# Performance work log

Hardware: AMD Instinct MI355X
Metric: run time of the kernel (lower is better)

## Reference

```python
import jax, jax.numpy as jnp
import numpy as np

B, U, T, H = 64, 64, 512, 8
N_NEIGHBORS = 8
NEG = -1e9

def setup_inputs() -> dict:
    key = jax.random.key(0)
    ks = jax.random.split(key, 12)
    f32 = jnp.float32
    def n(k, shp, s=1.0):
        return jax.random.normal(k, shp, dtype=f32) * s
    return {
        "usv_features": n(ks[0], (B, U, 4)),
        "task_features": n(ks[1], (B, T, 5)),
        "adj_matrix": jax.random.randint(ks[2], (B, U, T), 0, 2, dtype=jnp.int32),
        "edge_features": n(ks[3], (B, U, T, 1)),
        "W_usv": n(ks[4], (4, H), 0.3), "b_usv": jnp.zeros((H,), f32),
        "W_task": n(ks[5], (5, H), 0.3), "b_task": jnp.zeros((H,), f32),
        "W_au": n(ks[6], (H, 1), 0.3), "b_au": jnp.zeros((1,), f32),
        "W_at": n(ks[7], (H, 1), 0.3), "b_at": jnp.zeros((1,), f32),
        "W_Q": n(ks[8], (H, H), 0.3), "b_Q": jnp.zeros((H,), f32),
        "W_K": n(ks[9], (H, H), 0.3), "b_K": jnp.zeros((H,), f32),
        "W_V": n(ks[10], (H, H), 0.3), "b_V": jnp.zeros((H,), f32),
    }

def reference(usv_features, task_features, adj_matrix, edge_features,
              W_usv, b_usv, W_task, b_task, W_au, b_au, W_at, b_at,
              W_Q, b_Q, W_K, b_K, W_V, b_V):
    n_tasks = task_features.shape[1]
    # --- node encoders ---
    usv_embed = usv_features @ W_usv + b_usv        # [B,U,H]
    task_embed = task_features @ W_task + b_task    # [B,T,H]
    # --- USV <- Task additive attention ---
    uq = usv_embed @ W_Q + b_Q                      # [B,U,H]
    tk = task_embed @ W_K + b_K                     # [B,T,H]
    s = jnp.tanh(uq[:, :, None, :] + tk[:, None, :, :])  # [B,U,T,H]
    s = (s @ W_au + b_au)[..., 0]                   # [B,U,T]
    s = jnp.where(adj_matrix == 0, NEG, s)
    w = jax.nn.softmax(s, axis=-1)
    agg_task = jnp.einsum('but,bth->buh', w, task_embed)
    usv_self = jax.nn.sigmoid(uq)
    usv_updated = jax.nn.elu(usv_self * usv_embed + agg_task)  # [B,U,H]
    # --- Task <- Task kNN attention ---
    tq = task_embed @ W_V + b_V                     # [B,T,H]  (query via W_V as in source)
    coords = task_features[:, :, 0:2]
    diff = coords[:, :, None, :] - coords[:, None, :, :]
    dist = jnp.sqrt(jnp.sum(diff * diff, axis=-1))  # [B,T,T]  (torch.cdist p=2)
    k = min(N_NEIGHBORS + 1, n_tasks)
    _, idx = jax.lax.top_k(-dist, k)                # [B,T,k]
    task_adj = jnp.max(jax.nn.one_hot(idx, n_tasks, dtype=dist.dtype), axis=2)  # [B,T,T]
    ts = jnp.tanh(tq[:, :, None, :] + tk[:, None, :, :])  # [B,T,T,H]
    ts = (ts @ W_at + b_at)[..., 0]                 # [B,T,T]
    ts = jnp.where(task_adj == 0, NEG, ts)
    tw = jax.nn.softmax(ts, axis=-1)
    agg_tasks = jnp.einsum('bts,bsh->bth', tw, task_embed)
    # --- Task <- USV attention (softmax over USV axis) ---
    uk = usv_updated @ W_Q + b_Q                    # [B,U,H]
    tu = jnp.tanh(uk[:, :, None, :] + tq[:, None, :, :])  # [B,U,T,H]
    tu = (tu @ W_at + b_at)[..., 0]                 # [B,U,T]
    tuw = jax.nn.softmax(tu, axis=1)                # over USVs
    agg_usv = jnp.einsum('but,buh->bth', tuw, usv_updated)
    task_self = jax.nn.sigmoid(tq)
    task_updated = jax.nn.elu(task_self * task_embed + agg_tasks + agg_usv)
    return usv_updated, task_updated
```

## Files before the change

### kernel.cpp

```cpp
#include <hip/hip_runtime.h>
#include <hip/hip_bf16.h>

#define NB 64
#define NU 64
#define NT 512
#define NH 8
#define KNN 9
#define PAD 9
#define UPB 8
#define NEGV -1000000000.0f

typedef unsigned long long ull;

__device__ __forceinline__ float ft(float x) {
    return 1.f - 2.f / (__expf(2.f * x) + 1.f);
}

__global__ void __launch_bounds__(512) k_usv2(
    const float* __restrict__ usv_f, const float* __restrict__ task_f,
    const int* __restrict__ adj,
    const float* __restrict__ W_usv, const float* __restrict__ b_usv,
    const float* __restrict__ W_task, const float* __restrict__ b_task,
    const float* __restrict__ W_au, const float* __restrict__ b_au,
    const float* __restrict__ W_Q, const float* __restrict__ b_Q,
    const float* __restrict__ W_K, const float* __restrict__ b_K,
    float* __restrict__ out_usv)
{
    __shared__ float s_te[NT][PAD];
    __shared__ float s_p[NT];
    __shared__ float s_q[UPB][PAD];
    __shared__ float s_ue[UPB][PAD];
    __shared__ float s_mw[2][8];
    __shared__ float s_sw[2][8];
    __shared__ float s_wp[2][8][NH];

    const int b    = blockIdx.x >> 3;
    const int u0   = (blockIdx.x & 7) * UPB;
    const int t    = threadIdx.x;
    const int lane = t & 63, wv = t >> 6;

    float tkr[NH];
    {
        float f[5];
        #pragma unroll
        for (int j = 0; j < 5; ++j) f[j] = task_f[(b * NT + t) * 5 + j];
        float e[NH];
        #pragma unroll
        for (int h = 0; h < NH; ++h) {
            float a = b_task[h];
            #pragma unroll
            for (int j = 0; j < 5; ++j) a += f[j] * W_task[j * NH + h];
            e[h] = a;
            s_te[t][h] = a;
        }
        #pragma unroll
        for (int h = 0; h < NH; ++h) {
            float a = b_K[h];
            #pragma unroll
            for (int j = 0; j < NH; ++j) a += e[j] * W_K[j * NH + h];
            tkr[h] = a;
        }
    }
    if (t < UPB) {
        int u = u0 + t;
        float f0 = usv_f[(b * NU + u) * 4 + 0];
        float f1 = usv_f[(b * NU + u) * 4 + 1];
        float f2 = usv_f[(b * NU + u) * 4 + 2];
        float f3 = usv_f[(b * NU + u) * 4 + 3];
        float ue[NH];
        #pragma unroll
        for (int h = 0; h < NH; ++h) {
            ue[h] = b_usv[h] + f0 * W_usv[0 * NH + h] + f1 * W_usv[1 * NH + h]
                             + f2 * W_usv[2 * NH + h] + f3 * W_usv[3 * NH + h];
            s_ue[t][h] = ue[h];
        }
        #pragma unroll
        for (int h = 0; h < NH; ++h) {
            float a = b_Q[h];
            #pragma unroll
            for (int j = 0; j < NH; ++j) a += ue[j] * W_Q[j * NH + h];
            s_q[t][h] = a;
        }
    }
    float wau[NH];
    #pragma unroll
    for (int h = 0; h < NH; ++h) wau[h] = W_au[h];
    float bau = b_au[0];
    __syncthreads();

    for (int ui = 0; ui < UPB; ++ui) {
        const int par = ui & 1;
        const int u = u0 + ui;

        float sc = bau;
        #pragma unroll
        for (int h = 0; h < NH; ++h) sc += ft(s_q[ui][h] + tkr[h]) * wau[h];
        if (adj[(b * NU + u) * NT + t] == 0) sc = NEGV;

        float m = sc;
        #pragma unroll
        for (int o = 32; o; o >>= 1) m = fmaxf(m, __shfl_xor(m, o));
        float p = __expf(sc - m);
        s_p[t] = p;
        float ps = p;
        #pragma unroll
        for (int o = 32; o; o >>= 1) ps += __shfl_xor(ps, o);
        if (lane == 0) { s_mw[par][wv] = m; s_sw[par][wv] = ps; }

        const int g8 = t & ~7, hh = t & 7;
        float part = 0.f;
        #pragma unroll
        for (int i = 0; i < 8; ++i)
            part += s_p[g8 + i] * s_te[g8 + i][hh];
        part += __shfl_xor(part, 8);
        part += __shfl_xor(part, 16);
        part += __shfl_xor(part, 32);
        if (lane < NH) s_wp[par][wv][lane] = part;
        __syncthreads();

        if (t < NH) {
            float M = s_mw[par][0];
            #pragma unroll
            for (int w = 1; w < 8; ++w) M = fmaxf(M, s_mw[par][w]);
            float PS = 0.f, A = 0.f;
            #pragma unroll
            for (int w = 0; w < 8; ++w) {
                float ew = __expf(s_mw[par][w] - M);
                PS += s_sw[par][w] * ew;
                A  += s_wp[par][w][t] * ew;
            }
            float qh = s_q[ui][t], ueh = s_ue[ui][t];
            float sig = 1.f / (1.f + __expf(-qh));
            float x = sig * ueh + A / PS;
            float upd = x > 0.f ? x : __expf(x) - 1.f;
            out_usv[(b * NU + u) * NH + t] = upd;
        }
    }
}

__global__ void __launch_bounds__(512) k_task6(
    const float* __restrict__ task_f,
    const float* __restrict__ W_task, const float* __restrict__ b_task,
    const float* __restrict__ W_K, const float* __restrict__ b_K,
    const float* __restrict__ W_V, const float* __restrict__ b_V,
    const float* __restrict__ W_Q, const float* __restrict__ b_Q,
    const float* __restrict__ W_at, const float* __restrict__ b_at,
    const float* __restrict__ out_usv,
    float* __restrict__ out_task)
{
    __shared__ float2 s_cxy[NT];
    __shared__ float s_te[NT][PAD];
    __shared__ float s_tk[NT][PAD];
    __shared__ float s_up[NU][PAD];
    __shared__ float s_uk[NU][PAD];
    __shared__ int   s_nbi[8][8][KNN];
    __shared__ float s_p2[8][12];
    __shared__ float s_pu[8][NU];
    __shared__ float s_tq[8][PAD];

    const int b     = blockIdx.x >> 3;
    const int tile  = blockIdx.x & 7;
    const int wid   = threadIdx.x >> 6;
    const int lane  = threadIdx.x & 63;
    const int grp   = lane >> 3;
    const int lig   = lane & 7;
    const int tbase = tile * 64;
    const int myTask = tbase + wid * 8 + grp;

    {
        int i = threadIdx.x;
        float f[5];
        #pragma unroll
        for (int j = 0; j < 5; ++j) f[j] = task_f[(b * NT + i) * 5 + j];
        s_cxy[i] = make_float2(f[0], f[1]);
        float e[NH];
        #pragma unroll
        for (int h = 0; h < NH; ++h) {
            float a = b_task[h];
            #pragma unroll
            for (int j = 0; j < 5; ++j) a += f[j] * W_task[j * NH + h];
            e[h] = a;
            s_te[i][h] = a;
        }
        #pragma unroll
        for (int h = 0; h < NH; ++h) {
            float a = b_K[h];
            #pragma unroll
            for (int j = 0; j < NH; ++j) a += e[j] * W_K[j * NH + h];
            s_tk[i][h] = a;
        }
    }
    if (threadIdx.x < NU) {
        int u = threadIdx.x;
        float up[NH];
        #pragma unroll
        for (int h = 0; h < NH; ++h) {
            up[h] = out_usv[(b * NU + u) * NH + h];
            s_up[u][h] = up[h];
        }
        #pragma unroll
        for (int h = 0; h < NH; ++h) {
            float a = b_Q[h];
            #pragma unroll
            for (int j = 0; j < NH; ++j) a += up[j] * W_Q[j * NH + h];
            s_uk[u][h] = a;
        }
    }
    __syncthreads();

    {
        float mx = s_cxy[myTask].x, my = s_cxy[myTask].y;
        ull a[KNN];
        #pragma unroll
        for (int j = 0; j < KNN; ++j) a[j] = ~0ULL;
        for (int i = 0; i < 64; ++i) {
            int s = i * 8 + lig;
            float2 c = s_cxy[s];
            float dx = mx - c.x, dy = my - c.y;
            float d = sqrtf(dx * dx + dy * dy);
            ull k = ((ull)__float_as_uint(d) << 32) | (unsigned)s;
            bool cnd[KNN];
            #pragma unroll
            for (int j = 0; j < KNN; ++j) cnd[j] = k < a[j];
            #pragma unroll
            for (int j = KNN - 1; j >= 1; --j)
                a[j] = cnd[j] ? (cnd[j - 1] ? a[j - 1] : k) : a[j];
            a[0] = cnd[0] ? k : a[0];
        }
        #pragma unroll
        for (int r = 0; r < KNN; ++r) {
            ull m = a[0];
            #pragma unroll
            for (int o = 1; o <= 4; o <<= 1) {
                ull m2 = __shfl_xor(m, o);
                m = (m2 < m) ? m2 : m;
            }
            if (lig == 0) s_nbi[wid][grp][r] = (int)(m & 511ULL);
            bool won = (a[0] == m);
            #pragma unroll
            for (int j = 0; j < KNN - 1; ++j) a[j] = won ? a[j + 1] : a[j];
            a[KNN - 1] = won ? ~0ULL : a[KNN - 1];
        }
    }

    float wat[NH];
    #pragma unroll
    for (int h = 0; h < NH; ++h) wat[h] = W_at[h];
    const float bat = b_at[0];

    for (int g = 0; g < 8; ++g) {
        const int t = tbase + wid * 8 + g;
        const int mynb = (lane < KNN) ? s_nbi[wid][g][lane] : t;

        if (lane < NH) {
            float a = b_V[lane];
            #pragma unroll
            for (int j = 0; j < NH; ++j) a += s_te[t][j] * W_V[j * NH + lane];
            s_tq[wid][lane] = a;
        }

        float sc2 = bat;
        #pragma unroll
        for (int h = 0; h < NH; ++h)
            sc2 += ft(s_tq[wid][h] + s_tk[mynb][h]) * wat[h];
        float a2 = (lane < KNN) ? sc2 : -3.0e38f;
        float vm = a2;
        #pragma unroll
        for (int o = 8; o; o >>= 1) vm = fmaxf(vm, __shfl_xor(vm, o));
        float p2 = (lane < KNN) ? __expf(a2 - vm) : 0.f;
        float ss = p2;
        #pragma unroll
        for (int o = 8; o; o >>= 1) ss += __shfl_xor(ss, o);
        if (lane < KNN) s_p2[wid][lane] = p2;
        float aT = 0.f;
        if (lane < NH) {
            #pragma unroll
            for (int j2 = 0; j2 < KNN; ++j2)
                aT += s_p2[wid][j2] * s_te[s_nbi[wid][g][j2]][lane];
        }

        float au = bat;
        #pragma unroll
        for (int h = 0; h < NH; ++h)
            au += ft(s_uk[lane][h] + s_tq[wid][h]) * wat[h];
        float um = au;
        #pragma unroll
        for (int o = 32; o; o >>= 1) um = fmaxf(um, __shfl_xor(um, o));
        float pu = __expf(au - um);
        float su = pu;
        #pragma unroll
        for (int o = 32; o; o >>= 1) su += __shfl_xor(su, o);
        s_pu[wid][lane] = pu;
        const int gb = (lane >> 3) << 3;
        const int hh = lane & 7;
        float aU = 0.f;
        #pragma unroll
        for (int i = 0; i < 8; ++i)
            aU += s_pu[wid][gb + i] * s_up[gb + i][hh];
        aU += __shfl_xor(aU, 8);
        aU += __shfl_xor(aU, 16);
        aU += __shfl_xor(aU, 32);

        if (lane < NH) {
            float tqh = s_tq[wid][lane];
            float invT = 1.f / ss, invU = 1.f / su;
            float sig = 1.f / (1.f + __expf(-tqh));
            float x = sig * s_te[t][lane] + aT * invT + aU * invU;
            float r = x > 0.f ? x : __expf(x) - 1.f;
            out_task[(b * NT + t) * NH + lane] = r;
        }
    }
}

extern "C" void kernel_launch(void* const* d_in, const int* in_sizes, int n_in,
                              void* d_out, int out_size, void* d_ws, size_t ws_size,
                              hipStream_t stream)
{
    const float* usv_f  = (const float*)d_in[0];
    const float* task_f = (const float*)d_in[1];
    const int*   adj    = (const int*)  d_in[2];
    const float* W_usv  = (const float*)d_in[4];
    const float* b_usv  = (const float*)d_in[5];
    const float* W_task = (const float*)d_in[6];
    const float* b_task = (const float*)d_in[7];
    const float* W_au   = (const float*)d_in[8];
    const float* b_au   = (const float*)d_in[9];
    const float* W_at   = (const float*)d_in[10];
    const float* b_at   = (const float*)d_in[11];
    const float* W_Q    = (const float*)d_in[12];
    const float* b_Q    = (const float*)d_in[13];
    const float* W_K    = (const float*)d_in[14];
    const float* b_K    = (const float*)d_in[15];
    const float* W_V    = (const float*)d_in[16];
    const float* b_V    = (const float*)d_in[17];

    float* out_usv  = (float*)d_out;
    float* out_task = out_usv + NB * NU * NH;

    hipLaunchKernelGGL(k_usv2, dim3(NB * 8), dim3(512), 0, stream,
                       usv_f, task_f, adj,
                       W_usv, b_usv, W_task, b_task, W_au, b_au,
                       W_Q, b_Q, W_K, b_K, out_usv);
    hipLaunchKernelGGL(k_task6, dim3(NB * 8), dim3(512), 0, stream,
                       task_f, W_task, b_task, W_K, b_K, W_V, b_V,
                       W_Q, b_Q, W_at, b_at, out_usv, out_task);
}
```

Baseline: 83.89 us.

## Assign one USV per wavefront in usv attention kernel to drop block barriers

The USV-side attention kernel now maps each of the 8 wavefronts to one USV instead of looping over USVs with a block-wide barrier per iteration. Each wave processes all 512 tasks in 8 chunks of 64 lanes, computing max and sum with wave shuffles only. Task keys are staged in shared memory rather than held in registers. This removes seven __syncthreads and the cross-wave merge, in exchange for more LDS traffic and a per-wave shared-memory scratch for probabilities that relies on implicit wavefront lockstep.

```diff
diff --git a/kernel.cpp b/kernel.cpp
--- a/kernel.cpp
+++ b/kernel.cpp
@@ -16,7 +16,7 @@
     return 1.f - 2.f / (__expf(2.f * x) + 1.f);
 }
 
-__global__ void __launch_bounds__(512) k_usv2(
+__global__ void __launch_bounds__(512) k_usv3(
     const float* __restrict__ usv_f, const float* __restrict__ task_f,
     const int* __restrict__ adj,
     const float* __restrict__ W_usv, const float* __restrict__ b_usv,
@@ -27,20 +27,17 @@
     float* __restrict__ out_usv)
 {
     __shared__ float s_te[NT][PAD];
-    __shared__ float s_p[NT];
-    __shared__ float s_q[UPB][PAD];
-    __shared__ float s_ue[UPB][PAD];
-    __shared__ float s_mw[2][8];
-    __shared__ float s_sw[2][8];
-    __shared__ float s_wp[2][8][NH];
+    __shared__ float s_tk[NT][PAD];
+    __shared__ float s_p[8][NU];
 
     const int b    = blockIdx.x >> 3;
     const int u0   = (blockIdx.x & 7) * UPB;
-    const int t    = threadIdx.x;
-    const int lane = t & 63, wv = t >> 6;
-
-    float tkr[NH];
+    const int tid  = threadIdx.x;
+    const int lane = tid & 63, wid = tid >> 6;
+    const int u    = u0 + wid;
+
     {
+        int t = tid;
         float f[5];
         #pragma unroll
         for (int j = 0; j < 5; ++j) f[j] = task_f[(b * NT + t) * 5 + j];
@@ -58,83 +55,78 @@
             float a = b_K[h];
             #pragma unroll
             for (int j = 0; j < NH; ++j) a += e[j] * W_K[j * NH + h];
-            tkr[h] = a;
-        }
-    }
-    if (t < UPB) {
-        int u = u0 + t;
+            s_tk[t][h] = a;
+        }
+    }
+
+    float ue[NH], q[NH];
+    {
         float f0 = usv_f[(b * NU + u) * 4 + 0];
         float f1 = usv_f[(b * NU + u) * 4 + 1];
         float f2 = usv_f[(b * NU + u) * 4 + 2];
         float f3 = usv_f[(b * NU + u) * 4 + 3];
-        float ue[NH];
-        #pragma unroll
-        for (int h = 0; h < NH; ++h) {
+        #pragma unroll
+        for (int h = 0; h < NH; ++h)
             ue[h] = b_usv[h] + f0 * W_usv[0 * NH + h] + f1 * W_usv[1 * NH + h]
                              + f2 * W_usv[2 * NH + h] + f3 * W_usv[3 * NH + h];
-            s_ue[t][h] = ue[h];
-        }
         #pragma unroll
         for (int h = 0; h < NH; ++h) {
             float a = b_Q[h];
             #pragma unroll
             for (int j = 0; j < NH; ++j) a += ue[j] * W_Q[j * NH + h];
-            s_q[t][h] = a;
+            q[h] = a;
         }
     }
     float wau[NH];
     #pragma unroll
     for (int h = 0; h < NH; ++h) wau[h] = W_au[h];
-    float bau = b_au[0];
+    const float bau = b_au[0];
     __syncthreads();
 
-    for (int ui = 0; ui < UPB; ++ui) {
-        const int par = ui & 1;
-        const int u = u0 + ui;
-
-        float sc = bau;
-        #pragma unroll
-        for (int h = 0; h < NH; ++h) sc += ft(s_q[ui][h] + tkr[h]) * wau[h];
-        if (adj[(b * NU + u) * NT + t] == 0) sc = NEGV;
-
-        float m = sc;
-        #pragma unroll
-        for (int o = 32; o; o >>= 1) m = fmaxf(m, __shfl_xor(m, o));
-        float p = __expf(sc - m);
-        s_p[t] = p;
-        float ps = p;
-        #pragma unroll
-        for (int o = 32; o; o >>= 1) ps += __shfl_xor(ps, o);
-        if (lane == 0) { s_mw[par][wv] = m; s_sw[par][wv] = ps; }
-
-        const int g8 = t & ~7, hh = t & 7;
-        float part = 0.f;
-        #pragma unroll
-        for (int i = 0; i < 8; ++i)
-            part += s_p[g8 + i] * s_te[g8 + i][hh];
-        part += __shfl_xor(part, 8);
-        part += __shfl_xor(part, 16);
-        part += __shfl_xor(part, 32);
-        if (lane < NH) s_wp[par][wv][lane] = part;
-        __syncthreads();
-
-        if (t < NH) {
-            float M = s_mw[par][0];
-            #pragma unroll
-            for (int w = 1; w < 8; ++w) M = fmaxf(M, s_mw[par][w]);
-            float PS = 0.f, A = 0.f;
-            #pragma unroll
-            for (int w = 0; w < 8; ++w) {
-                float ew = __expf(s_mw[par][w] - M);
-                PS += s_sw[par][w] * ew;
-                A  += s_wp[par][w][t] * ew;
-            }
-            float qh = s_q[ui][t], ueh = s_ue[ui][t];
-            float sig = 1.f / (1.f + __expf(-qh));
-            float x = sig * ueh + A / PS;
-            float upd = x > 0.f ? x : __expf(x) - 1.f;
-            out_usv[(b * NU + u) * NH + t] = upd;
-        }
+    const int* arow = adj + (b * NU + u) * NT;
+
+    float sc[8];
+    float m = -3.0e38f;
+    #pragma unroll
+    for (int i = 0; i < 8; ++i) {
+        int t = i * 64 + lane;
+        float a = bau;
+        #pragma unroll
+        for (int h = 0; h < NH; ++h) a += ft(q[h] + s_tk[t][h]) * wau[h];
+        sc[i] = (arow[t] == 0) ? NEGV : a;
+        m = fmaxf(m, sc[i]);
+    }
+    #pragma unroll
+    for (int o = 32; o; o >>= 1) m = fmaxf(m, __shfl_xor(m, o));
+
+    const int g8 = lane & ~7, hh = lane & 7;
+    float ps = 0.f, part = 0.f;
+    #pragma unroll
+    for (int i = 0; i < 8; ++i) {
+        float p = __expf(sc[i] - m);
+        ps += p;
+        s_p[wid][lane] = p;
+        float acc = 0.f;
+        #pragma unroll
+        for (int k = 0; k < 8; ++k)
+            acc += s_p[wid][g8 + k] * s_te[i * 64 + g8 + k][hh];
+        part += acc;
+    }
+    #pragma unroll
+    for (int o = 32; o; o >>= 1) ps += __shfl_xor(ps, o);
+    part += __shfl_xor(part, 8);
+    part += __shfl_xor(part, 16);
+    part += __shfl_xor(part, 32);
+
+    if (lane < NH) {
+        float qh = q[0], ueh = ue[0];
+        #pragma unroll
+        for (int h = 1; h < NH; ++h)
+            if (lane == h) { qh = q[h]; ueh = ue[h]; }
+        float sig = 1.f / (1.f + __expf(-qh));
+        float x = sig * ueh + part / ps;
+        float upd = x > 0.f ? x : __expf(x) - 1.f;
+        out_usv[(b * NU + u) * NH + lane] = upd;
     }
 }
 
@@ -337,7 +329,7 @@
     float* out_usv  = (float*)d_out;
     float* out_task = out_usv + NB * NU * NH;
 
-    hipLaunchKernelGGL(k_usv2, dim3(NB * 8), dim3(512), 0, stream,
+    hipLaunchKernelGGL(k_usv3, dim3(NB * 8), dim3(512), 0, stream,
                        usv_f, task_f, adj,
                        W_usv, b_usv, W_task, b_task, W_au, b_au,
                        W_Q, b_Q, W_K, b_K, out_usv);
```

New measurement: 78.91 us. 5.9% less time.
